# Kernel tuning notes

Measured on AMD Instinct MI355X. Metric: run time of the kernel, lower is better.

## Reference

```python
import jax, jax.numpy as jnp
import numpy as np

B, N, C = 8, 16384, 40
E, KD, VD = 512, 256, 256


def setup_inputs() -> dict:
    key = jax.random.key(0)
    ks = jax.random.split(key, 10)
    s = 0.02
    return {
        "q": jax.random.normal(ks[0], (B, N, E), jnp.float32),
        "k": jax.random.normal(ks[1], (B, C, KD), jnp.float32),
        "v": jax.random.normal(ks[2], (B, C, VD), jnp.float32),
        "coarse_pred": jax.random.normal(ks[3], (B, C, N), jnp.float32),
        "Wq": jax.random.normal(ks[4], (E, E), jnp.float32) * s,
        "bq": jnp.zeros((E,), jnp.float32),
        "Wk": jax.random.normal(ks[5], (E, KD), jnp.float32) * s,
        "bk": jnp.zeros((E,), jnp.float32),
        "Wv": jax.random.normal(ks[6], (E, VD), jnp.float32) * s,
        "bv": jnp.zeros((E,), jnp.float32),
    }


def reference(q, k, v, coarse_pred, Wq, bq, Wk, bk, Wv, bv):
    # Projections (nn.Linear: x @ W.T + b)
    qp = jnp.einsum("bne,fe->bnf", q, Wq) + bq          # (B, N, E)
    kp = jnp.einsum("bcd,fd->bcf", k, Wk) + bk          # (B, C, E)
    vp = jnp.einsum("bcd,fd->bcf", v, Wv) + bv          # (B, C, E)

    scale = 1.0 / jnp.sqrt(jnp.float32(E))
    attn = jnp.einsum("bne,bce->bnc", qp, kp) * scale   # (B, N, C)
    attn = jax.nn.softmax(attn, axis=-1)

    # coarse_pred is detached, transposed to (B, N, C), softmaxed over classes
    cp = jax.nn.softmax(jnp.swapaxes(coarse_pred, 1, 2), axis=-1)
    attn = jax.nn.softmax(attn * cp, axis=-1)

    out = jnp.einsum("bnc,bce->bne", attn, vp)          # (B, N, E)
    return out
```

## Files before the change

### kernel.cpp

```cpp
#include <hip/hip_runtime.h>
#include <hip/hip_bf16.h>
#include <stdint.h>

#define Bb 8
#define Nn 16384
#define Cc 40
#define Ee 512
#define Dd 256

typedef __attribute__((ext_vector_type(4))) float f32x4;
typedef __attribute__((ext_vector_type(8))) short bf16x8;

__device__ __forceinline__ unsigned short f2bf(float f) {
  union { float f; uint32_t u; } x; x.f = f;
  uint32_t r = x.u + 0x7FFFu + ((x.u >> 16) & 1u);
  return (unsigned short)(r >> 16);
}
__device__ __forceinline__ unsigned int pack2(float a, float b) {
  return (unsigned int)f2bf(a) | ((unsigned int)f2bf(b) << 16);
}
__device__ __forceinline__ bf16x8 q2bf(float4 a, float4 c) {
  union { __hip_bfloat162 h2[4]; bf16x8 v; } u;
  u.h2[0] = __float22bfloat162_rn(float2{a.x, a.y});
  u.h2[1] = __float22bfloat162_rn(float2{a.z, a.w});
  u.h2[2] = __float22bfloat162_rn(float2{c.x, c.y});
  u.h2[3] = __float22bfloat162_rn(float2{c.z, c.w});
  return u.v;
}

__global__ __launch_bounds__(256) void prepA_kernel(
    const float* __restrict__ Wq, const float* __restrict__ Wk,
    const float* __restrict__ bq, const float* __restrict__ bk,
    float* __restrict__ Mt, float* __restrict__ tvec,
    float* __restrict__ uvec, float* __restrict__ bqbk) {
  const int t = threadIdx.x;
  if (blockIdx.x == 8) {
    if (blockIdx.z != 0) return;
    const int by = blockIdx.y;
    if (by < 2) {
      const int e = by * 256 + t;
      float s = 0.f;
      #pragma unroll 8
      for (int f = 0; f < Ee; f++) s += Wq[(size_t)f * Ee + e] * bk[f];
      tvec[e] = s;
    } else if (by == 2) {
      const int d = t;
      float s = 0.f;
      #pragma unroll 8
      for (int f = 0; f < Ee; f++) s += Wk[(size_t)f * Dd + d] * bq[f];
      uvec[d] = s;
    } else {
      __shared__ float red[256];
      float p = 0.f;
      for (int f = t; f < Ee; f += 256) p += bq[f] * bk[f];
      red[t] = p; __syncthreads();
      #pragma unroll
      for (int off = 128; off > 0; off >>= 1) {
        if (t < off) red[t] += red[t + off];
        __syncthreads();
      }
      if (t == 0) bqbk[0] = red[0];
    }
    return;
  }
  __shared__ float WqL[64][68];
  __shared__ float WkL[64][68];
  const int te = (t & 15) * 4;
  const int td = (t >> 4) * 4;
  const int ebase = blockIdx.x * 64, dbase = blockIdx.y * 64;
  const int fbase = blockIdx.z * 256;
  f32x4 acc0 = {0,0,0,0}, acc1 = {0,0,0,0}, acc2 = {0,0,0,0}, acc3 = {0,0,0,0};
  for (int f0 = 0; f0 < 256; f0 += 64) {
    __syncthreads();
    #pragma unroll
    for (int i = 0; i < 4; i++) {
      int idx = t + i * 256;
      int row = idx >> 4, c4 = (idx & 15) * 4;
      *(float4*)&WqL[row][c4] = *(const float4*)(Wq + (size_t)(fbase + f0 + row) * Ee + ebase + c4);
      *(float4*)&WkL[row][c4] = *(const float4*)(Wk + (size_t)(fbase + f0 + row) * Dd + dbase + c4);
    }
    __syncthreads();
    #pragma unroll 8
    for (int ff = 0; ff < 64; ff++) {
      float4 a = *(const float4*)&WkL[ff][td];
      float4 b = *(const float4*)&WqL[ff][te];
      acc0[0] += a.x*b.x; acc0[1] += a.x*b.y; acc0[2] += a.x*b.z; acc0[3] += a.x*b.w;
      acc1[0] += a.y*b.x; acc1[1] += a.y*b.y; acc1[2] += a.y*b.z; acc1[3] += a.y*b.w;
      acc2[0] += a.z*b.x; acc2[1] += a.z*b.y; acc2[2] += a.z*b.z; acc2[3] += a.z*b.w;
      acc3[0] += a.w*b.x; acc3[1] += a.w*b.y; acc3[2] += a.w*b.z; acc3[3] += a.w*b.w;
    }
  }
  float* mt = Mt + (size_t)blockIdx.z * 131072;
  *(f32x4*)&mt[(size_t)(dbase + td + 0) * Ee + ebase + te] = acc0;
  *(f32x4*)&mt[(size_t)(dbase + td + 1) * Ee + ebase + te] = acc1;
  *(f32x4*)&mt[(size_t)(dbase + td + 2) * Ee + ebase + te] = acc2;
  *(f32x4*)&mt[(size_t)(dbase + td + 3) * Ee + ebase + te] = acc3;
}

__global__ __launch_bounds__(256) void prepB_kernel(
    const float* __restrict__ k, const float* __restrict__ v,
    const float* __restrict__ Wv, const float* __restrict__ bv,
    const float* __restrict__ Mt, const float* __restrict__ tvec,
    const float* __restrict__ uvec, const float* __restrict__ bqbk,
    unsigned short* __restrict__ abf, unsigned short* __restrict__ vpf,
    float* __restrict__ dbias) {
  __shared__ float xL[8][Dd];
  const int t = threadIdx.x;
  const int el = t & 127, half = t >> 7;
  const int e = blockIdx.y * 128 + el;

  if (blockIdx.x < 48) {
    const int sbase = blockIdx.x * 8;
    for (int i = t; i < 8 * Dd; i += 256) {
      int row = i >> 8, dd = i & (Dd - 1);
      int sg = sbase + row, bb_ = sg / 48, cc = sg % 48;
      xL[row][dd] = (cc < 40) ? k[((size_t)bb_ * Cc + cc) * Dd + dd] : 0.f;
    }
    __syncthreads();
    float acc[4] = {0,0,0,0};
    float db[4]  = {0,0,0,0};
    #pragma unroll 8
    for (int d = 0; d < Dd; d++) {
      float mt = Mt[(size_t)d * Ee + e] + Mt[131072 + (size_t)d * Ee + e];
      float ud = uvec[d];
      #pragma unroll
      for (int si = 0; si < 4; si++) {
        float kv = xL[half*4 + si][d];
        acc[si] += mt * kv;
        db[si]  += ud * kv;
      }
    }
    const float scale = 0.044194173824159216f;
    const float te = tvec[e];
    const float bqbkv = bqbk[0];
    const int ks = e >> 5, gg = (e >> 3) & 3, j = e & 7;
    #pragma unroll
    for (int si = 0; si < 4; si++) {
      int sg = sbase + half*4 + si, bb_ = sg / 48, cc = sg % 48;
      int ct = cc >> 4, lane16 = (cc & 15) + 16*gg;
      unsigned short val = (cc < 40) ? f2bf(scale * (acc[si] + te)) : (unsigned short)0;
      abf[((((size_t)bb_*3 + ct)*16 + ks)*64 + lane16)*8 + j] = val;
      if (el == 0) dbias[bb_*64 + cc] = (cc < 40) ? scale * (db[si] + bqbkv) : 0.f;
    }
  } else {
    const int sbase = (blockIdx.x - 48) * 8;
    for (int i = t; i < 8 * Dd; i += 256) {
      int row = i >> 8, dd = i & (Dd - 1);
      int sg = sbase + row, bb_ = sg >> 6, cc = sg & 63;
      xL[row][dd] = (cc < 40) ? v[((size_t)bb_ * Cc + cc) * Dd + dd] : 0.f;
    }
    __syncthreads();
    const float* wrow = Wv + (size_t)e * Dd;
    float acc[4] = {0,0,0,0};
    #pragma unroll 2
    for (int dd = 0; dd < Dd; dd += 4) {
      float4 w = *(const float4*)(wrow + dd);
      #pragma unroll
      for (int si = 0; si < 4; si++) {
        float4 vv = *(const float4*)&xL[half*4 + si][dd];
        acc[si] += w.x*vv.x + w.y*vv.y + w.z*vv.z + w.w*vv.w;
      }
    }
    const float bve = bv[e];
    const int nt = e >> 4, elan = e & 15;
    #pragma unroll
    for (int si = 0; si < 4; si++) {
      int sg = sbase + half*4 + si, bb_ = sg >> 6, cc = sg & 63;
      int s = cc >> 5, gg = (cc >> 3) & 3, j = cc & 7;
      unsigned short val = (cc < 40) ? f2bf(acc[si] + bve) : (unsigned short)0;
      vpf[((((size_t)bb_*32 + nt)*2 + s)*64 + (elan + 16*gg))*8 + j] = val;
    }
  }
}

__global__ __launch_bounds__(512) void main_kernel(
    const float* __restrict__ q, const float* __restrict__ coarse,
    const unsigned short* __restrict__ abfrag,
    const unsigned short* __restrict__ vpfrag,
    const float* __restrict__ dbias, float* __restrict__ out) {
  __shared__ uint4 fragL[7168];
  __shared__ unsigned short s_att[8][16][72];
  const int t = threadIdx.x;
  const int wave = t >> 6, lane = t & 63;
  const int r = lane & 15, g = lane >> 4;
  const int b = blockIdx.x >> 5;
  const int seg = blockIdx.x & 31;
  const bool v2 = (g < 2);

  {
    const uint4* srcA = (const uint4*)abfrag + (size_t)b * 3072;
    #pragma unroll
    for (int i = 0; i < 6; i++) fragL[t + i*512] = srcA[t + i*512];
    const uint4* srcV = (const uint4*)vpfrag + (size_t)b * 4096;
    #pragma unroll
    for (int i = 0; i < 8; i++) fragL[3072 + t + i*512] = srcV[t + i*512];
  }
  __syncthreads();

  const int row0 = seg * 512 + wave * 16;
  const float* qrow0 = q + ((size_t)b * Nn + row0 + r) * Ee + 8 * g;
  const float* cbase0 = coarse + (size_t)b * Cc * Nn + row0 + r;
  float* outb0 = out + ((size_t)b * Nn + row0 + r) * Ee + 4 * g;

  for (int it = 0; it < 4; it++) {
    const float* qr = qrow0 + (size_t)(it*128) * Ee;
    f32x4 acc0 = {0,0,0,0}, acc1 = {0,0,0,0}, acc2 = {0,0,0,0};

    float4 a0, a1, a2, a3, b0, b1, b2, b3;
    auto LD_A = [&](int c) {
      a0 = *(const float4*)(qr + 64*c);
      a1 = *(const float4*)(qr + 64*c + 4);
      a2 = *(const float4*)(qr + 64*c + 32);
      a3 = *(const float4*)(qr + 64*c + 36);
    };
    auto LD_B = [&](int c) {
      b0 = *(const float4*)(qr + 64*c);
      b1 = *(const float4*)(qr + 64*c + 4);
      b2 = *(const float4*)(qr + 64*c + 32);
      b3 = *(const float4*)(qr + 64*c + 36);
    };
    auto MM = [&](int c, float4 x0, float4 x1, float4 x2, float4 x3) {
      bf16x8 q0 = q2bf(x0, x1), q1 = q2bf(x2, x3);
      const int ks = 2*c;
      acc0 = __builtin_amdgcn_mfma_f32_16x16x32_bf16(*(const bf16x8*)&fragL[(0*16+ks)*64 + lane], q0, acc0, 0,0,0);
      acc1 = __builtin_amdgcn_mfma_f32_16x16x32_bf16(*(const bf16x8*)&fragL[(1*16+ks)*64 + lane], q0, acc1, 0,0,0);
      acc2 = __builtin_amdgcn_mfma_f32_16x16x32_bf16(*(const bf16x8*)&fragL[(2*16+ks)*64 + lane], q0, acc2, 0,0,0);
      acc0 = __builtin_amdgcn_mfma_f32_16x16x32_bf16(*(const bf16x8*)&fragL[(0*16+ks+1)*64 + lane], q1, acc0, 0,0,0);
      acc1 = __builtin_amdgcn_mfma_f32_16x16x32_bf16(*(const bf16x8*)&fragL[(1*16+ks+1)*64 + lane], q1, acc1, 0,0,0);
      acc2 = __builtin_amdgcn_mfma_f32_16x16x32_bf16(*(const bf16x8*)&fragL[(2*16+ks+1)*64 + lane], q1, acc2, 0,0,0);
    };

    LD_A(0);
    LD_B(1);

    const float* cb = cbase0 + it*128;
    float cr[3][4];
    #pragma unroll
    for (int rg = 0; rg < 4; rg++) {
      cr[0][rg] = cb[(size_t)( 0 + 4*g + rg) * Nn];
      cr[1][rg] = cb[(size_t)(16 + 4*g + rg) * Nn];
      cr[2][rg] = v2 ? cb[(size_t)(32 + 4*g + rg) * Nn] : -3e38f;
    }

    MM(0, a0,a1,a2,a3); LD_A(2);
    MM(1, b0,b1,b2,b3); LD_B(3);
    MM(2, a0,a1,a2,a3); LD_A(4);
    MM(3, b0,b1,b2,b3); LD_B(5);
    MM(4, a0,a1,a2,a3); LD_A(6);
    MM(5, b0,b1,b2,b3); LD_B(7);
    MM(6, a0,a1,a2,a3);
    MM(7, b0,b1,b2,b3);

    const float4 db0 = *(const float4*)(dbias + b*64 +  0 + 4*g);
    const float4 db1 = *(const float4*)(dbias + b*64 + 16 + 4*g);
    const float4 db2 = *(const float4*)(dbias + b*64 + 32 + 4*g);

    float x[3][4];
    #pragma unroll
    for (int rg = 0; rg < 4; rg++) {
      x[0][rg] = acc0[rg] + ((const float*)&db0)[rg];
      x[1][rg] = acc1[rg] + ((const float*)&db1)[rg];
      x[2][rg] = acc2[rg] + ((const float*)&db2)[rg];
    }

    float m1 = -3e38f;
    #pragma unroll
    for (int rg = 0; rg < 4; rg++) {
      m1 = fmaxf(m1, x[0][rg]); m1 = fmaxf(m1, x[1][rg]);
      if (v2) m1 = fmaxf(m1, x[2][rg]);
    }
    m1 = fmaxf(m1, __shfl_xor(m1, 16));
    m1 = fmaxf(m1, __shfl_xor(m1, 32));
    float s1 = 0.f;
    #pragma unroll
    for (int rg = 0; rg < 4; rg++) {
      x[0][rg] = __expf(x[0][rg] - m1); s1 += x[0][rg];
      x[1][rg] = __expf(x[1][rg] - m1); s1 += x[1][rg];
      x[2][rg] = v2 ? __expf(x[2][rg] - m1) : 0.f; s1 += x[2][rg];
    }
    s1 += __shfl_xor(s1, 16); s1 += __shfl_xor(s1, 32);

    float m2 = -3e38f;
    #pragma unroll
    for (int rg = 0; rg < 4; rg++) {
      m2 = fmaxf(m2, cr[0][rg]); m2 = fmaxf(m2, cr[1][rg]);
      if (v2) m2 = fmaxf(m2, cr[2][rg]);
    }
    m2 = fmaxf(m2, __shfl_xor(m2, 16));
    m2 = fmaxf(m2, __shfl_xor(m2, 32));
    float s2 = 0.f;
    #pragma unroll
    for (int rg = 0; rg < 4; rg++) {
      cr[0][rg] = __expf(cr[0][rg] - m2); s2 += cr[0][rg];
      cr[1][rg] = __expf(cr[1][rg] - m2); s2 += cr[1][rg];
      cr[2][rg] = v2 ? __expf(cr[2][rg] - m2) : 0.f; s2 += cr[2][rg];
    }
    s2 += __shfl_xor(s2, 16); s2 += __shfl_xor(s2, 32);

    const float sc12 = 1.0f / (s1 * s2);
    float m3 = -3e38f;
    #pragma unroll
    for (int rg = 0; rg < 4; rg++) {
      x[0][rg] *= cr[0][rg] * sc12;
      x[1][rg] *= cr[1][rg] * sc12;
      x[2][rg] = v2 ? (x[2][rg] * cr[2][rg] * sc12) : 0.f;
      m3 = fmaxf(m3, x[0][rg]); m3 = fmaxf(m3, x[1][rg]);
      if (v2) m3 = fmaxf(m3, x[2][rg]);
    }
    m3 = fmaxf(m3, __shfl_xor(m3, 16));
    m3 = fmaxf(m3, __shfl_xor(m3, 32));
    float s3 = 0.f;
    #pragma unroll
    for (int rg = 0; rg < 4; rg++) {
      x[0][rg] = __expf(x[0][rg] - m3); s3 += x[0][rg];
      x[1][rg] = __expf(x[1][rg] - m3); s3 += x[1][rg];
      x[2][rg] = v2 ? __expf(x[2][rg] - m3) : 0.f; s3 += x[2][rg];
    }
    s3 += __shfl_xor(s3, 16); s3 += __shfl_xor(s3, 32);
    const float inv3 = 1.0f / s3;

    unsigned int* srow = (unsigned int*)&s_att[wave][r][0];
    #pragma unroll
    for (int ct = 0; ct < 3; ct++) {
      srow[8*ct + 2*g + 0] = pack2(x[ct][0]*inv3, x[ct][1]*inv3);
      srow[8*ct + 2*g + 1] = pack2(x[ct][2]*inv3, x[ct][3]*inv3);
    }
    srow[24 + 2*g + 0] = 0u;
    srow[24 + 2*g + 1] = 0u;
    asm volatile("s_waitcnt lgkmcnt(0)" ::: "memory");
    const bf16x8 pa0 = *(const bf16x8*)&s_att[wave][r][ 0 + 8*g];
    const bf16x8 pa1 = *(const bf16x8*)&s_att[wave][r][32 + 8*g];

    float* outp = outb0 + (size_t)(it*128) * Ee;
    #pragma unroll 8
    for (int nt = 0; nt < 32; nt++) {
      bf16x8 vf0 = *(const bf16x8*)&fragL[3072 + (nt*2 + 0)*64 + lane];
      bf16x8 vf1 = *(const bf16x8*)&fragL[3072 + (nt*2 + 1)*64 + lane];
      f32x4 o = {0,0,0,0};
      o = __builtin_amdgcn_mfma_f32_16x16x32_bf16(vf0, pa0, o, 0,0,0);
      o = __builtin_amdgcn_mfma_f32_16x16x32_bf16(vf1, pa1, o, 0,0,0);
      *(f32x4*)(outp + nt*16) = o;
    }
  }
}

extern "C" void kernel_launch(void* const* d_in, const int* in_sizes, int n_in,
                              void* d_out, int out_size, void* d_ws, size_t ws_size,
                              hipStream_t stream) {
  const float* q   = (const float*)d_in[0];
  const float* k   = (const float*)d_in[1];
  const float* v   = (const float*)d_in[2];
  const float* cps = (const float*)d_in[3];
  const float* Wq  = (const float*)d_in[4];
  const float* bq  = (const float*)d_in[5];
  const float* Wk  = (const float*)d_in[6];
  const float* bk  = (const float*)d_in[7];
  const float* Wv  = (const float*)d_in[8];
  const float* bv  = (const float*)d_in[9];
  float* out = (float*)d_out;
  char* ws = (char*)d_ws;

  float*          Mt    = (float*)(ws);
  float*          tvec  = (float*)(ws + 1048576);
  float*          uvec  = (float*)(ws + 1050624);
  float*          bqbkp = (float*)(ws + 1051648);
  unsigned short* abf   = (unsigned short*)(ws + 1052672);
  unsigned short* vpf   = (unsigned short*)(ws + 1052672 + 393216);
  float*          dbias = (float*)(ws + 1052672 + 393216 + 524288);

  prepA_kernel<<<dim3(9, 4, 2), 256, 0, stream>>>(Wq, Wk, bq, bk, Mt, tvec, uvec, bqbkp);
  prepB_kernel<<<dim3(112, 4),  256, 0, stream>>>(k, v, Wv, bv, Mt, tvec, uvec, bqbkp,
                                                  abf, vpf, dbias);
  main_kernel <<<dim3(256),     512, 0, stream>>>(q, cps, abf, vpf, dbias, out);
}
```

Baseline: 173.8 us.

## Stage q tiles through swizzled LDS for coalesced loads before MFMA projection

New measurement: 215.0 us. +23.7%, slower.

```diff
diff --git a/kernel.cpp b/kernel.cpp
--- a/kernel.cpp
+++ b/kernel.cpp
@@ -18,14 +18,6 @@
 }
 __device__ __forceinline__ unsigned int pack2(float a, float b) {
   return (unsigned int)f2bf(a) | ((unsigned int)f2bf(b) << 16);
-}
-__device__ __forceinline__ bf16x8 q2bf(float4 a, float4 c) {
-  union { __hip_bfloat162 h2[4]; bf16x8 v; } u;
-  u.h2[0] = __float22bfloat162_rn(float2{a.x, a.y});
-  u.h2[1] = __float22bfloat162_rn(float2{a.z, a.w});
-  u.h2[2] = __float22bfloat162_rn(float2{c.x, c.y});
-  u.h2[3] = __float22bfloat162_rn(float2{c.z, c.w});
-  return u.v;
 }
 
 __global__ __launch_bounds__(256) void prepA_kernel(
@@ -179,13 +171,15 @@
     const unsigned short* __restrict__ vpfrag,
     const float* __restrict__ dbias, float* __restrict__ out) {
   __shared__ uint4 fragL[7168];
-  __shared__ unsigned short s_att[8][16][72];
+  __shared__ unsigned short qstg[8][16][128];
   const int t = threadIdx.x;
   const int wave = t >> 6, lane = t & 63;
   const int r = lane & 15, g = lane >> 4;
   const int b = blockIdx.x >> 5;
   const int seg = blockIdx.x & 31;
   const bool v2 = (g < 2);
+  const int srow = lane >> 5;
+  const int sc16 = lane & 31;
 
   {
     const uint4* srcA = (const uint4*)abfrag + (size_t)b * 3072;
@@ -197,43 +191,54 @@
   }
   __syncthreads();
 
-  const int row0 = seg * 512 + wave * 16;
-  const float* qrow0 = q + ((size_t)b * Nn + row0 + r) * Ee + 8 * g;
-  const float* cbase0 = coarse + (size_t)b * Cc * Nn + row0 + r;
-  float* outb0 = out + ((size_t)b * Nn + row0 + r) * Ee + 4 * g;
+  char* const qw = (char*)&qstg[wave][0][0];
 
   for (int it = 0; it < 4; it++) {
-    const float* qr = qrow0 + (size_t)(it*128) * Ee;
+    const int rowit = seg * 512 + it * 128 + wave * 16;
+    const float* qb = q + ((size_t)b * Nn + rowit) * Ee + sc16 * 4;
     f32x4 acc0 = {0,0,0,0}, acc1 = {0,0,0,0}, acc2 = {0,0,0,0};
 
-    float4 a0, a1, a2, a3, b0, b1, b2, b3;
-    auto LD_A = [&](int c) {
-      a0 = *(const float4*)(qr + 64*c);
-      a1 = *(const float4*)(qr + 64*c + 4);
-      a2 = *(const float4*)(qr + 64*c + 32);
-      a3 = *(const float4*)(qr + 64*c + 36);
+    float4 gA[4], gB[4];
+    auto LOADG_A = [&](int qt) {
+      #pragma unroll
+      for (int i = 0; i < 4; i++)
+        gA[i] = *(const float4*)(qb + (size_t)(2*i + srow) * Ee + qt*128);
     };
-    auto LD_B = [&](int c) {
-      b0 = *(const float4*)(qr + 64*c);
-      b1 = *(const float4*)(qr + 64*c + 4);
-      b2 = *(const float4*)(qr + 64*c + 32);
-      b3 = *(const float4*)(qr + 64*c + 36);
+    auto LOADG_B = [&](int qt) {
+      #pragma unroll
+      for (int i = 0; i < 4; i++)
+        gB[i] = *(const float4*)(qb + (size_t)(8 + 2*i + srow) * Ee + qt*128);
     };
-    auto MM = [&](int c, float4 x0, float4 x1, float4 x2, float4 x3) {
-      bf16x8 q0 = q2bf(x0, x1), q1 = q2bf(x2, x3);
-      const int ks = 2*c;
-      acc0 = __builtin_amdgcn_mfma_f32_16x16x32_bf16(*(const bf16x8*)&fragL[(0*16+ks)*64 + lane], q0, acc0, 0,0,0);
-      acc1 = __builtin_amdgcn_mfma_f32_16x16x32_bf16(*(const bf16x8*)&fragL[(1*16+ks)*64 + lane], q0, acc1, 0,0,0);
-      acc2 = __builtin_amdgcn_mfma_f32_16x16x32_bf16(*(const bf16x8*)&fragL[(2*16+ks)*64 + lane], q0, acc2, 0,0,0);
-      acc0 = __builtin_amdgcn_mfma_f32_16x16x32_bf16(*(const bf16x8*)&fragL[(0*16+ks+1)*64 + lane], q1, acc0, 0,0,0);
-      acc1 = __builtin_amdgcn_mfma_f32_16x16x32_bf16(*(const bf16x8*)&fragL[(1*16+ks+1)*64 + lane], q1, acc1, 0,0,0);
-      acc2 = __builtin_amdgcn_mfma_f32_16x16x32_bf16(*(const bf16x8*)&fragL[(2*16+ks+1)*64 + lane], q1, acc2, 0,0,0);
+    auto CVTWR = [&](const float4* G, int rbase) {
+      #pragma unroll
+      for (int i = 0; i < 4; i++) {
+        const int row = rbase + 2*i + srow;
+        uint2 hv;
+        hv.x = pack2(G[i].x, G[i].y);
+        hv.y = pack2(G[i].z, G[i].w);
+        const int off = (sc16 * 8) ^ ((row & 7) << 4);
+        *(uint2*)(qw + row*256 + off) = hv;
+      }
     };
-
-    LD_A(0);
-    LD_B(1);
-
-    const float* cb = cbase0 + it*128;
+    auto COMPUTE = [&](int qt) {
+      #pragma unroll
+      for (int kl = 0; kl < 4; kl++) {
+        const int off = (64*kl + 16*g) ^ ((r & 7) << 4);
+        bf16x8 qf = *(const bf16x8*)(qw + r*256 + off);
+        const int ks = 4*qt + kl;
+        acc0 = __builtin_amdgcn_mfma_f32_16x16x32_bf16(*(const bf16x8*)&fragL[(0*16+ks)*64 + lane], qf, acc0, 0,0,0);
+        acc1 = __builtin_amdgcn_mfma_f32_16x16x32_bf16(*(const bf16x8*)&fragL[(1*16+ks)*64 + lane], qf, acc1, 0,0,0);
+        acc2 = __builtin_amdgcn_mfma_f32_16x16x32_bf16(*(const bf16x8*)&fragL[(2*16+ks)*64 + lane], qf, acc2, 0,0,0);
+      }
+    };
+
+    LOADG_A(0); LOADG_B(0);
+    CVTWR(gA, 0); CVTWR(gB, 8); LOADG_A(1); LOADG_B(1); COMPUTE(0);
+    CVTWR(gA, 0); CVTWR(gB, 8); LOADG_A(2); LOADG_B(2); COMPUTE(1);
+    CVTWR(gA, 0); CVTWR(gB, 8); LOADG_A(3); LOADG_B(3); COMPUTE(2);
+    CVTWR(gA, 0); CVTWR(gB, 8);                         COMPUTE(3);
+
+    const float* cb = coarse + (size_t)b * Cc * Nn + rowit + r;
     float cr[3][4];
     #pragma unroll
     for (int rg = 0; rg < 4; rg++) {
@@ -241,15 +246,6 @@
       cr[1][rg] = cb[(size_t)(16 + 4*g + rg) * Nn];
       cr[2][rg] = v2 ? cb[(size_t)(32 + 4*g + rg) * Nn] : -3e38f;
     }
-
-    MM(0, a0,a1,a2,a3); LD_A(2);
-    MM(1, b0,b1,b2,b3); LD_B(3);
-    MM(2, a0,a1,a2,a3); LD_A(4);
-    MM(3, b0,b1,b2,b3); LD_B(5);
-    MM(4, a0,a1,a2,a3); LD_A(6);
-    MM(5, b0,b1,b2,b3); LD_B(7);
-    MM(6, a0,a1,a2,a3);
-    MM(7, b0,b1,b2,b3);
 
     const float4 db0 = *(const float4*)(dbias + b*64 +  0 + 4*g);
     const float4 db1 = *(const float4*)(dbias + b*64 + 16 + 4*g);
@@ -319,19 +315,20 @@
     s3 += __shfl_xor(s3, 16); s3 += __shfl_xor(s3, 32);
     const float inv3 = 1.0f / s3;
 
-    unsigned int* srow = (unsigned int*)&s_att[wave][r][0];
+    unsigned short (*sa)[72] = (unsigned short (*)[72])qw;
+    unsigned int* srowp = (unsigned int*)&sa[r][0];
     #pragma unroll
     for (int ct = 0; ct < 3; ct++) {
-      srow[8*ct + 2*g + 0] = pack2(x[ct][0]*inv3, x[ct][1]*inv3);
-      srow[8*ct + 2*g + 1] = pack2(x[ct][2]*inv3, x[ct][3]*inv3);
-    }
-    srow[24 + 2*g + 0] = 0u;
-    srow[24 + 2*g + 1] = 0u;
+      srowp[8*ct + 2*g + 0] = pack2(x[ct][0]*inv3, x[ct][1]*inv3);
+      srowp[8*ct + 2*g + 1] = pack2(x[ct][2]*inv3, x[ct][3]*inv3);
+    }
+    srowp[24 + 2*g + 0] = 0u;
+    srowp[24 + 2*g + 1] = 0u;
     asm volatile("s_waitcnt lgkmcnt(0)" ::: "memory");
-    const bf16x8 pa0 = *(const bf16x8*)&s_att[wave][r][ 0 + 8*g];
-    const bf16x8 pa1 = *(const bf16x8*)&s_att[wave][r][32 + 8*g];
-
-    float* outp = outb0 + (size_t)(it*128) * Ee;
+    const bf16x8 pa0 = *(const bf16x8*)&sa[r][ 0 + 8*g];
+    const bf16x8 pa1 = *(const bf16x8*)&sa[r][32 + 8*g];
+
+    float* outp = out + ((size_t)b * Nn + rowit + r) * Ee + 4 * g;
     #pragma unroll 8
     for (int nt = 0; nt < 32; nt++) {
       bf16x8 vf0 = *(const bf16x8*)&fragL[3072 + (nt*2 + 0)*64 + lane];
```
